# Kernel tuning notes

Hardware: AMD Instinct MI355X
Metric: run time of the kernel (lower is better)

## Reference

```python
import jax, jax.numpy as jnp
import numpy as np

DIM = 512
QK_DIM = 128
HIDDEN = 1024


def setup_inputs() -> dict:
    key = jax.random.key(0)
    ks = jax.random.split(key, 8)
    b, n = 4, 4096
    x = jax.random.normal(ks[0], (b, n, DIM), dtype=jnp.float32)
    # nn.Linear(dim, hidden*2)
    w_hidden = jax.random.normal(ks[1], (DIM, 2 * HIDDEN), dtype=jnp.float32) / np.sqrt(DIM)
    b_hidden = jnp.zeros((2 * HIDDEN,), dtype=jnp.float32)
    # nn.Linear(dim, qk_dim, bias=False)
    w_qk = jax.random.normal(ks[2], (DIM, QK_DIM), dtype=jnp.float32) / np.sqrt(DIM)
    # OffsetScale params (gamma init 1, beta init 0; randomize slightly for a nontrivial test)
    q_gamma = 1.0 + 0.02 * jax.random.normal(ks[3], (QK_DIM,), dtype=jnp.float32)
    q_beta = 0.02 * jax.random.normal(ks[4], (QK_DIM,), dtype=jnp.float32)
    k_gamma = 1.0 + 0.02 * jax.random.normal(ks[5], (QK_DIM,), dtype=jnp.float32)
    k_beta = 0.02 * jax.random.normal(ks[6], (QK_DIM,), dtype=jnp.float32)
    # nn.Linear(hidden, dim)
    w_out = jax.random.normal(ks[7], (HIDDEN, DIM), dtype=jnp.float32) / np.sqrt(HIDDEN)
    b_out = jnp.zeros((DIM,), dtype=jnp.float32)
    return {
        "x": x,
        "w_hidden": w_hidden, "b_hidden": b_hidden,
        "w_qk": w_qk,
        "q_gamma": q_gamma, "q_beta": q_beta,
        "k_gamma": k_gamma, "k_beta": k_beta,
        "w_out": w_out, "b_out": b_out,
    }


def reference(x, w_hidden, b_hidden, w_qk, q_gamma, q_beta, k_gamma, k_beta, w_out, b_out):
    scale = QK_DIM ** -0.5
    # to_hidden -> chunk into v, gate (NOTE: source applies no activation here)
    hid = jnp.einsum('bnd,dh->bnh', x, w_hidden) + b_hidden  # [b, n, 2*hidden]
    v, gate = jnp.split(hid, 2, axis=-1)                     # each [b, n, hidden]
    qk = jnp.einsum('bnd,de->bne', x, w_qk)                  # [b, n, qk_dim]
    q = qk * q_gamma + q_beta
    k = qk * k_gamma + k_beta
    sim = jnp.einsum('bid,bjd->bij', q, k) * scale           # [b, n, n]
    attn = jnp.square(jax.nn.relu(sim))                      # ReLU^2, no softmax
    out = jnp.einsum('bij,bjh->bih', attn, v)                # [b, n, hidden]
    out = out * gate
    out = jnp.einsum('bnh,hd->bnd', out, w_out) + b_out      # [b, n, dim]
    return out + x  # add_residual=True
```

## Files before the change

### kernel.cpp

```cpp
#include <hip/hip_runtime.h>
#include <hip/hip_bf16.h>

typedef __attribute__((ext_vector_type(8))) short bf16x8;
typedef __attribute__((ext_vector_type(4))) float f32x4;
typedef unsigned short u16;

__device__ __forceinline__ u16 f2b(float f) {
  __hip_bfloat16 h = __float2bfloat16(f);
  return __builtin_bit_cast(unsigned short, h);
}
__device__ __forceinline__ float b2f(u16 u) {
  __hip_bfloat16 h = __builtin_bit_cast(__hip_bfloat16, u);
  return __bfloat162float(h);
}

#define BAR() __builtin_amdgcn_s_barrier()
#define LGKM0() do { asm volatile("s_waitcnt lgkmcnt(0)" ::: "memory"); __builtin_amdgcn_sched_barrier(0); } while (0)
#define LGKM4() do { asm volatile("s_waitcnt lgkmcnt(4)" ::: "memory"); __builtin_amdgcn_sched_barrier(0); } while (0)
#define LGKM8() do { asm volatile("s_waitcnt lgkmcnt(8)" ::: "memory"); __builtin_amdgcn_sched_barrier(0); } while (0)
#define VMCNT4() asm volatile("s_waitcnt vmcnt(4)" ::: "memory")
#define VMCNT2() asm volatile("s_waitcnt vmcnt(2)" ::: "memory")
#define VMCNT0() asm volatile("s_waitcnt vmcnt(0)" ::: "memory")

#define EPI_HID 0
#define EPI_QK 1
#define EPI_ATTN 2
#define EPI_PV 3
#define EPI_OUT 4

__device__ __forceinline__ void stage_tile(char* sbase, const char* gbase, int ld_bytes, int tid) {
#pragma unroll
  for (int i = 0; i < 4; ++i) {
    int o = (i * 256 + tid) * 16;
    int row = o >> 7;
    int cb = o & 127;
    int scb = cb ^ ((row & 7) << 4);
    const char* src = gbase + (long)row * ld_bytes + scb;
    __builtin_amdgcn_global_load_lds((const __attribute__((address_space(1))) void*)src,
                                     (__attribute__((address_space(3))) void*)(sbase + o),
                                     16, 0, 0);
  }
}

template <int EPI>
__global__ __launch_bounds__(256, 2) void gemm_tn(
    const char* Ab, const char* Bb, long sAbat, long sBbat,
    int lda_b, int ldb_b, int nkt,
    u16* o0, u16* o1,
    const float* a0, const float* a1, const float* a2, const float* a3,
    float* fout, const float* xres) {
  __shared__ __align__(16) char lds[32768];
  char* sA = lds;
  char* sB = lds + 16384;
  const int tid = threadIdx.x;
  const int lane = tid & 63;
  const int wave = tid >> 6;
  const int wm = wave >> 1, wn = wave & 1;
  const int l16 = lane & 15, lq = lane >> 4;
  const int bat = blockIdx.z;
  const int row0 = blockIdx.y * 128;
  const int col0 = blockIdx.x * 128;

  const char* Abase = Ab + (long)bat * sAbat + (long)row0 * lda_b;
  const char* Bbase = Bb + (long)bat * sBbat + (long)col0 * ldb_b;

  f32x4 acc[4][4];
#pragma unroll
  for (int i = 0; i < 4; ++i)
#pragma unroll
    for (int j = 0; j < 4; ++j) acc[i][j] = (f32x4){0.f, 0.f, 0.f, 0.f};

  for (int kt = 0; kt < nkt; ++kt) {
    stage_tile(sA, Abase + (long)kt * 128, lda_b, tid);
    stage_tile(sB, Bbase + (long)kt * 128, ldb_b, tid);
    __syncthreads();
#pragma unroll
    for (int kk = 0; kk < 2; ++kk) {
      bf16x8 af[4], bfr[4];
#pragma unroll
      for (int mf = 0; mf < 4; ++mf) {
        int r = wm * 64 + mf * 16 + l16;
        int kb = kk * 64 + lq * 16;
        af[mf] = *(const bf16x8*)(sA + r * 128 + (kb ^ ((r & 7) << 4)));
      }
#pragma unroll
      for (int nf = 0; nf < 4; ++nf) {
        int r = wn * 64 + nf * 16 + l16;
        int kb = kk * 64 + lq * 16;
        bfr[nf] = *(const bf16x8*)(sB + r * 128 + (kb ^ ((r & 7) << 4)));
      }
#pragma unroll
      for (int mf = 0; mf < 4; ++mf)
#pragma unroll
        for (int nf = 0; nf < 4; ++nf)
          acc[mf][nf] = __builtin_amdgcn_mfma_f32_16x16x32_bf16(af[mf], bfr[nf], acc[mf][nf], 0, 0, 0);
    }
    __syncthreads();
  }

#pragma unroll
  for (int mf = 0; mf < 4; ++mf) {
#pragma unroll
    for (int nf = 0; nf < 4; ++nf) {
      const int row = row0 + wm * 64 + mf * 16 + lq * 4;
      const int col = col0 + wn * 64 + nf * 16 + l16;
      f32x4 v = acc[mf][nf];
      if constexpr (EPI == EPI_QK) {
        float qg = a0[col], qbt = a1[col], kg = a2[col], kbt = a3[col];
#pragma unroll
        for (int i = 0; i < 4; ++i) {
          float t = v[i];
          o0[(size_t)(row + i) * 128 + col] = f2b(t * qg + qbt);
          o1[(size_t)(row + i) * 128 + col] = f2b(t * kg + kbt);
        }
      }
    }
  }
}

__device__ __forceinline__ void stage_half(char* sbase, const char* gbase, long ld, int tid) {
#pragma unroll
  for (int i = 0; i < 2; ++i) {
    int o = (i * 512 + tid) * 16;
    int row = o >> 7;
    int cb = o & 127;
    int scb = cb ^ ((row & 7) << 4);
    const char* src = gbase + (long)row * ld + scb;
    __builtin_amdgcn_global_load_lds((const __attribute__((address_space(1))) void*)src,
                                     (__attribute__((address_space(3))) void*)(sbase + o),
                                     16, 0, 0);
  }
}

template <int EPI>
__global__ __launch_bounds__(512, 2) void gemm256(
    const char* Ab, const char* Bb, long sAbat, long sBbat,
    long lda, long ldb, int nkt, int nx,
    u16* o0, u16* o1,
    const float* a0, float* fout, const float* xres) {
  extern __shared__ __align__(16) char lds[];
  const int tid = threadIdx.x;
  const int lane = tid & 63;
  const int wave = tid >> 6;
  const int wm = wave >> 2;
  const int wn = wave & 3;
  const int l16 = lane & 15, lq = lane >> 4;
  const int bat = blockIdx.y;

  const int nwg = gridDim.x;
  const int qq = nwg >> 3;
  const int fid = blockIdx.x;
  const int swz = (fid & 7) * qq + (fid >> 3);
  const int row0 = (swz / nx) * 256;
  const int col0 = (swz % nx) * 256;

  const char* gA = Ab + (long)bat * sAbat + (long)row0 * lda;
  const char* gB = Bb + (long)bat * sBbat + (long)col0 * ldb;

  f32x4 acc[8][4];
#pragma unroll
  for (int i = 0; i < 8; ++i)
#pragma unroll
    for (int j = 0; j < 4; ++j) acc[i][j] = (f32x4){0.f, 0.f, 0.f, 0.f};

  const int kmask = (l16 & 7) << 4;
  const int kb0 = (lq * 16) ^ kmask;
  const int kb1 = (64 + lq * 16) ^ kmask;
  const int rB = (wn & 1) * 64;

  stage_half(lds + 32768, gB, ldb, tid);
  stage_half(lds + 32768 + 16384, gB + 128 * ldb, ldb, tid);
  stage_half(lds, gA, lda, tid);
  stage_half(lds + 16384, gA + 128 * lda, lda, tid);
  if (nkt > 1) {
    stage_half(lds + 65536 + 32768, gB + 128, ldb, tid);
    stage_half(lds + 65536 + 32768 + 16384, gB + 128 * ldb + 128, ldb, tid);
    VMCNT4();
  } else {
    VMCNT0();
  }
  BAR();

  bf16x8 af0[4], af1[4], afp0[4], afp1[4], bfr0[4], bfr1[4];
  {
    const char* myA = lds + wm * 16384;
    const char* myB = lds + 32768 + (wn >> 1) * 16384;
#pragma unroll
    for (int nf = 0; nf < 4; ++nf)
      bfr0[nf] = *(const bf16x8*)(myB + (rB + nf * 16 + l16) * 128 + kb0);
#pragma unroll
    for (int mf = 0; mf < 4; ++mf)
      af0[mf] = *(const bf16x8*)(myA + (mf * 16 + l16) * 128 + kb0);
  }

  for (int t = 0; t < nkt; ++t) {
    const char* bufc = lds + (t & 1) * 65536;
    const char* bufn = lds + ((t + 1) & 1) * 65536;
    const char* myA = bufc + wm * 16384;
    const char* myB = bufc + 32768 + (wn >> 1) * 16384;
    const char* nA = bufn + wm * 16384;
    const char* nB = bufn + 32768 + (wn >> 1) * 16384;
    char* stA = (char*)bufn;
    char* stB = (char*)bufc + 32768;
    const bool sA_ok = (t + 1) < nkt;
    const bool sB_ok = (t + 2) < nkt;

#pragma unroll
    for (int nf = 0; nf < 4; ++nf)
      bfr1[nf] = *(const bf16x8*)(myB + (rB + nf * 16 + l16) * 128 + kb1);
#pragma unroll
    for (int mf = 0; mf < 4; ++mf)
      af1[mf] = *(const bf16x8*)(myA + (mf * 16 + l16) * 128 + kb1);
    if (sA_ok) stage_half(stA, gA + (long)(t + 1) * 128, lda, tid);
    LGKM8();
    __builtin_amdgcn_s_setprio(1);
#pragma unroll
    for (int mf = 0; mf < 4; ++mf)
#pragma unroll
      for (int nf = 0; nf < 4; ++nf)
        acc[mf][nf] = __builtin_amdgcn_mfma_f32_16x16x32_bf16(af0[mf], bfr0[nf], acc[mf][nf], 0, 0, 0);
    __builtin_amdgcn_s_setprio(0);

#pragma unroll
    for (int mf = 0; mf < 4; ++mf)
      afp0[mf] = *(const bf16x8*)(myA + (64 + mf * 16 + l16) * 128 + kb0);
    if (sA_ok) stage_half(stA + 16384, gA + 128 * lda + (long)(t + 1) * 128, lda, tid);
    LGKM4();
    __builtin_amdgcn_s_setprio(1);
#pragma unroll
    for (int mf = 0; mf < 4; ++mf)
#pragma unroll
      for (int nf = 0; nf < 4; ++nf)
        acc[mf][nf] = __builtin_amdgcn_mfma_f32_16x16x32_bf16(af1[mf], bfr1[nf], acc[mf][nf], 0, 0, 0);
    __builtin_amdgcn_s_setprio(0);
    BAR();

#pragma unroll
    for (int mf = 0; mf < 4; ++mf)
      afp1[mf] = *(const bf16x8*)(myA + (64 + mf * 16 + l16) * 128 + kb1);
    if (sB_ok) stage_half(stB, gB + (long)(t + 2) * 128, ldb, tid);
    LGKM4();
    __builtin_amdgcn_s_setprio(1);
#pragma unroll
    for (int mf = 0; mf < 4; ++mf)
#pragma unroll
      for (int nf = 0; nf < 4; ++nf)
        acc[4 + mf][nf] = __builtin_amdgcn_mfma_f32_16x16x32_bf16(afp0[mf], bfr0[nf], acc[4 + mf][nf], 0, 0, 0);
    __builtin_amdgcn_s_setprio(0);
    if (sA_ok) {
      if (sB_ok) { VMCNT2(); } else { VMCNT0(); }
      BAR();
    }

    if (sA_ok) {
#pragma unroll
      for (int nf = 0; nf < 4; ++nf)
        bfr0[nf] = *(const bf16x8*)(nB + (rB + nf * 16 + l16) * 128 + kb0);
#pragma unroll
      for (int mf = 0; mf < 4; ++mf)
        af0[mf] = *(const bf16x8*)(nA + (mf * 16 + l16) * 128 + kb0);
    }
    if (sB_ok) stage_half(stB + 16384, gB + 128 * ldb + (long)(t + 2) * 128, ldb, tid);
    if (sA_ok) { LGKM8(); } else { LGKM0(); }
    __builtin_amdgcn_s_setprio(1);
#pragma unroll
    for (int mf = 0; mf < 4; ++mf)
#pragma unroll
      for (int nf = 0; nf < 4; ++nf)
        acc[4 + mf][nf] = __builtin_amdgcn_mfma_f32_16x16x32_bf16(afp1[mf], bfr1[nf], acc[4 + mf][nf], 0, 0, 0);
    __builtin_amdgcn_s_setprio(0);
    BAR();
  }

#pragma unroll
  for (int mi = 0; mi < 8; ++mi) {
#pragma unroll
    for (int ni = 0; ni < 4; ++ni) {
      const int row = row0 + wm * 128 + mi * 16 + lq * 4;
      const int col = col0 + wn * 64 + ni * 16 + l16;
      f32x4 v = acc[mi][ni];
      if constexpr (EPI == EPI_HID) {
        float bias = a0[col];
        u16* dst = (col < 1024) ? (o0 + (size_t)col * 16384 + row)
                                : (o1 + (size_t)(col - 1024) * 16384 + row);
        *(ushort4*)dst = make_ushort4(f2b(v.x + bias), f2b(v.y + bias), f2b(v.z + bias), f2b(v.w + bias));
      } else if constexpr (EPI == EPI_ATTN) {
        const float scale = 0.088388347648318447f;
        u16* dst = o0 + (size_t)bat * 4096 * 4096;
#pragma unroll
        for (int i = 0; i < 4; ++i) {
          float t = v[i] * scale;
          t = t > 0.f ? t * t : 0.f;
          dst[(size_t)(row + i) * 4096 + col] = f2b(t);
        }
      } else if constexpr (EPI == EPI_PV) {
        const u16* gt = o1 + (size_t)col * 16384 + (size_t)bat * 4096 + row;
        ushort4 g = *(const ushort4*)gt;
        u16* dst = o0 + (size_t)bat * 4096 * 1024;
        dst[(size_t)(row + 0) * 1024 + col] = f2b(v.x * b2f(g.x));
        dst[(size_t)(row + 1) * 1024 + col] = f2b(v.y * b2f(g.y));
        dst[(size_t)(row + 2) * 1024 + col] = f2b(v.z * b2f(g.z));
        dst[(size_t)(row + 3) * 1024 + col] = f2b(v.w * b2f(g.w));
      } else if constexpr (EPI == EPI_OUT) {
        float bias = a0[col];
#pragma unroll
        for (int i = 0; i < 4; ++i)
          fout[(size_t)(row + i) * 512 + col] = v[i] + bias + xres[(size_t)(row + i) * 512 + col];
      }
    }
  }
}

__global__ void conv_b(const float* in, u16* out, int n) {
  int i = (blockIdx.x * blockDim.x + threadIdx.x) * 4;
  if (i >= n) return;
  float4 f = *(const float4*)(in + i);
  *(ushort4*)(out + i) = make_ushort4(f2b(f.x), f2b(f.y), f2b(f.z), f2b(f.w));
}

__global__ void transpose_b(const float* in, u16* out, int R, int C) {
  int o = blockIdx.x * blockDim.x + threadIdx.x;
  if (o >= R * C) return;
  int c = o / R, r = o - c * R;
  out[o] = f2b(in[(size_t)r * C + c]);
}

extern "C" void kernel_launch(void* const* d_in, const int* in_sizes, int n_in,
                              void* d_out, int out_size, void* d_ws, size_t ws_size,
                              hipStream_t stream) {
  const float* x = (const float*)d_in[0];
  const float* w_hidden = (const float*)d_in[1];
  const float* b_hidden = (const float*)d_in[2];
  const float* w_qk = (const float*)d_in[3];
  const float* q_gamma = (const float*)d_in[4];
  const float* q_beta = (const float*)d_in[5];
  const float* k_gamma = (const float*)d_in[6];
  const float* k_beta = (const float*)d_in[7];
  const float* w_out = (const float*)d_in[8];
  const float* b_out = (const float*)d_in[9];
  float* out = (float*)d_out;

  char* ws = (char*)d_ws;
  size_t off = 0;
  auto alloc = [&](size_t bytes) { char* p = ws + off; off += (bytes + 255) & ~255ull; return p; };
  u16* xb     = (u16*)alloc(16384ull * 512 * 2);
  u16* wh_t   = (u16*)alloc(2048ull * 512 * 2);
  u16* wqk_t  = (u16*)alloc(128ull * 512 * 2);
  u16* wout_t = (u16*)alloc(512ull * 1024 * 2);
  u16* v_t    = (u16*)alloc(1024ull * 16384 * 2);
  u16* g_t    = (u16*)alloc(1024ull * 16384 * 2);
  u16* qb_a   = (u16*)alloc(16384ull * 128 * 2);
  u16* kb_a   = (u16*)alloc(16384ull * 128 * 2);
  u16* attnb  = (u16*)alloc(4ull * 4096 * 4096 * 2);
  u16* out1b  = (u16*)alloc(16384ull * 1024 * 2);

  (void)hipFuncSetAttribute((const void*)gemm256<EPI_HID>, hipFuncAttributeMaxDynamicSharedMemorySize, 131072);
  (void)hipFuncSetAttribute((const void*)gemm256<EPI_ATTN>, hipFuncAttributeMaxDynamicSharedMemorySize, 131072);
  (void)hipFuncSetAttribute((const void*)gemm256<EPI_PV>, hipFuncAttributeMaxDynamicSharedMemorySize, 131072);
  (void)hipFuncSetAttribute((const void*)gemm256<EPI_OUT>, hipFuncAttributeMaxDynamicSharedMemorySize, 131072);

  conv_b<<<(16384 * 512 / 4 + 255) / 256, 256, 0, stream>>>(x, xb, 16384 * 512);
  transpose_b<<<(512 * 2048 + 255) / 256, 256, 0, stream>>>(w_hidden, wh_t, 512, 2048);
  transpose_b<<<(512 * 128 + 255) / 256, 256, 0, stream>>>(w_qk, wqk_t, 512, 128);
  transpose_b<<<(1024 * 512 + 255) / 256, 256, 0, stream>>>(w_out, wout_t, 1024, 512);

  gemm256<EPI_HID><<<dim3(512, 1), 512, 131072, stream>>>(
      (const char*)xb, (const char*)wh_t, 0, 0, 1024, 1024, 8, 8,
      v_t, g_t, b_hidden, nullptr, nullptr);
  gemm_tn<EPI_QK><<<dim3(1, 128, 1), 256, 0, stream>>>(
      (const char*)xb, (const char*)wqk_t, 0, 0, 1024, 1024, 8,
      qb_a, kb_a, q_gamma, q_beta, k_gamma, k_beta, nullptr, nullptr);
  gemm256<EPI_ATTN><<<dim3(256, 4), 512, 131072, stream>>>(
      (const char*)qb_a, (const char*)kb_a, 4096ll * 256, 4096ll * 256, 256, 256, 2, 16,
      attnb, nullptr, nullptr, nullptr, nullptr);
  gemm256<EPI_PV><<<dim3(64, 4), 512, 131072, stream>>>(
      (const char*)attnb, (const char*)v_t, 4096ll * 8192, 8192, 8192, 32768, 64, 4,
      out1b, g_t, nullptr, nullptr, nullptr);
  gemm256<EPI_OUT><<<dim3(128, 1), 512, 131072, stream>>>(
      (const char*)out1b, (const char*)wout_t, 0, 0, 2048, 2048, 16, 2,
      nullptr, nullptr, b_out, out, x);
}
```

Measured before the change: 343.7 us.

## Switch 256-tile GEMM to 32x32x16 MFMA and move output projection to gemm_tn

Rewrites the main 256x256 GEMM inner loop to use 32x32x16 bf16 MFMA instructions with 16-float accumulators instead of 16x16x32, which halves the instruction count per tile and changes the fragment layout and epilogue indexing. It also moves the final output-projection GEMM to the smaller gemm_tn kernel with a new EPI_OUT epilogue, giving more workgroups for that small-N problem. The risks are new LDS bank-conflict patterns from the different fragment layout and changed register pressure.

```diff
diff --git a/kernel.cpp b/kernel.cpp
--- a/kernel.cpp
+++ b/kernel.cpp
@@ -3,6 +3,7 @@
 
 typedef __attribute__((ext_vector_type(8))) short bf16x8;
 typedef __attribute__((ext_vector_type(4))) float f32x4;
+typedef __attribute__((ext_vector_type(16))) float f32x16;
 typedef unsigned short u16;
 
 __device__ __forceinline__ u16 f2b(float f) {
@@ -113,6 +114,11 @@
           o0[(size_t)(row + i) * 128 + col] = f2b(t * qg + qbt);
           o1[(size_t)(row + i) * 128 + col] = f2b(t * kg + kbt);
         }
+      } else if constexpr (EPI == EPI_OUT) {
+        float bias = a0[col];
+#pragma unroll
+        for (int i = 0; i < 4; ++i)
+          fout[(size_t)(row + i) * 512 + col] = v[i] + bias + xres[(size_t)(row + i) * 512 + col];
       }
     }
   }
@@ -144,7 +150,7 @@
   const int wave = tid >> 6;
   const int wm = wave >> 2;
   const int wn = wave & 3;
-  const int l16 = lane & 15, lq = lane >> 4;
+  const int l31 = lane & 31, hi = lane >> 5;
   const int bat = blockIdx.y;
 
   const int nwg = gridDim.x;
@@ -157,15 +163,18 @@
   const char* gA = Ab + (long)bat * sAbat + (long)row0 * lda;
   const char* gB = Bb + (long)bat * sBbat + (long)col0 * ldb;
 
-  f32x4 acc[8][4];
-#pragma unroll
-  for (int i = 0; i < 8; ++i)
-#pragma unroll
-    for (int j = 0; j < 4; ++j) acc[i][j] = (f32x4){0.f, 0.f, 0.f, 0.f};
-
-  const int kmask = (l16 & 7) << 4;
-  const int kb0 = (lq * 16) ^ kmask;
-  const int kb1 = (64 + lq * 16) ^ kmask;
+  f32x16 acc[4][2];
+#pragma unroll
+  for (int i = 0; i < 4; ++i)
+#pragma unroll
+    for (int j = 0; j < 2; ++j)
+#pragma unroll
+      for (int e = 0; e < 16; ++e) acc[i][j][e] = 0.f;
+
+  const int kmask = (l31 & 7) << 4;
+  int kb[4];
+#pragma unroll
+  for (int ks = 0; ks < 4; ++ks) kb[ks] = (ks * 32 + hi * 16) ^ kmask;
   const int rB = (wn & 1) * 64;
 
   stage_half(lds + 32768, gB, ldb, tid);
@@ -186,11 +195,15 @@
     const char* myA = lds + wm * 16384;
     const char* myB = lds + 32768 + (wn >> 1) * 16384;
 #pragma unroll
-    for (int nf = 0; nf < 4; ++nf)
-      bfr0[nf] = *(const bf16x8*)(myB + (rB + nf * 16 + l16) * 128 + kb0);
-#pragma unroll
-    for (int mf = 0; mf < 4; ++mf)
-      af0[mf] = *(const bf16x8*)(myA + (mf * 16 + l16) * 128 + kb0);
+    for (int ni = 0; ni < 2; ++ni)
+#pragma unroll
+      for (int ki = 0; ki < 2; ++ki)
+        bfr0[ni * 2 + ki] = *(const bf16x8*)(myB + (rB + ni * 32 + l31) * 128 + kb[ki]);
+#pragma unroll
+    for (int mi = 0; mi < 2; ++mi)
+#pragma unroll
+      for (int ki = 0; ki < 2; ++ki)
+        af0[mi * 2 + ki] = *(const bf16x8*)(myA + (mi * 32 + l31) * 128 + kb[ki]);
   }
 
   for (int t = 0; t < nkt; ++t) {
@@ -206,46 +219,60 @@
     const bool sB_ok = (t + 2) < nkt;
 
 #pragma unroll
-    for (int nf = 0; nf < 4; ++nf)
-      bfr1[nf] = *(const bf16x8*)(myB + (rB + nf * 16 + l16) * 128 + kb1);
-#pragma unroll
-    for (int mf = 0; mf < 4; ++mf)
-      af1[mf] = *(const bf16x8*)(myA + (mf * 16 + l16) * 128 + kb1);
+    for (int ni = 0; ni < 2; ++ni)
+#pragma unroll
+      for (int ki = 0; ki < 2; ++ki)
+        bfr1[ni * 2 + ki] = *(const bf16x8*)(myB + (rB + ni * 32 + l31) * 128 + kb[2 + ki]);
+#pragma unroll
+    for (int mi = 0; mi < 2; ++mi)
+#pragma unroll
+      for (int ki = 0; ki < 2; ++ki)
+        af1[mi * 2 + ki] = *(const bf16x8*)(myA + (mi * 32 + l31) * 128 + kb[2 + ki]);
     if (sA_ok) stage_half(stA, gA + (long)(t + 1) * 128, lda, tid);
     LGKM8();
     __builtin_amdgcn_s_setprio(1);
 #pragma unroll
-    for (int mf = 0; mf < 4; ++mf)
-#pragma unroll
-      for (int nf = 0; nf < 4; ++nf)
-        acc[mf][nf] = __builtin_amdgcn_mfma_f32_16x16x32_bf16(af0[mf], bfr0[nf], acc[mf][nf], 0, 0, 0);
+    for (int ki = 0; ki < 2; ++ki)
+#pragma unroll
+      for (int mi = 0; mi < 2; ++mi)
+#pragma unroll
+        for (int ni = 0; ni < 2; ++ni)
+          acc[mi][ni] = __builtin_amdgcn_mfma_f32_32x32x16_bf16(af0[mi * 2 + ki], bfr0[ni * 2 + ki], acc[mi][ni], 0, 0, 0);
     __builtin_amdgcn_s_setprio(0);
 
 #pragma unroll
-    for (int mf = 0; mf < 4; ++mf)
-      afp0[mf] = *(const bf16x8*)(myA + (64 + mf * 16 + l16) * 128 + kb0);
+    for (int mi = 0; mi < 2; ++mi)
+#pragma unroll
+      for (int ki = 0; ki < 2; ++ki)
+        afp0[mi * 2 + ki] = *(const bf16x8*)(myA + ((mi + 2) * 32 + l31) * 128 + kb[ki]);
     if (sA_ok) stage_half(stA + 16384, gA + 128 * lda + (long)(t + 1) * 128, lda, tid);
     LGKM4();
     __builtin_amdgcn_s_setprio(1);
 #pragma unroll
-    for (int mf = 0; mf < 4; ++mf)
-#pragma unroll
-      for (int nf = 0; nf < 4; ++nf)
-        acc[mf][nf] = __builtin_amdgcn_mfma_f32_16x16x32_bf16(af1[mf], bfr1[nf], acc[mf][nf], 0, 0, 0);
+    for (int ki = 0; ki < 2; ++ki)
+#pragma unroll
+      for (int mi = 0; mi < 2; ++mi)
+#pragma unroll
+        for (int ni = 0; ni < 2; ++ni)
+          acc[mi][ni] = __builtin_amdgcn_mfma_f32_32x32x16_bf16(af1[mi * 2 + ki], bfr1[ni * 2 + ki], acc[mi][ni], 0, 0, 0);
     __builtin_amdgcn_s_setprio(0);
     BAR();
 
 #pragma unroll
-    for (int mf = 0; mf < 4; ++mf)
-      afp1[mf] = *(const bf16x8*)(myA + (64 + mf * 16 + l16) * 128 + kb1);
+    for (int mi = 0; mi < 2; ++mi)
+#pragma unroll
+      for (int ki = 0; ki < 2; ++ki)
+        afp1[mi * 2 + ki] = *(const bf16x8*)(myA + ((mi + 2) * 32 + l31) * 128 + kb[2 + ki]);
     if (sB_ok) stage_half(stB, gB + (long)(t + 2) * 128, ldb, tid);
     LGKM4();
     __builtin_amdgcn_s_setprio(1);
 #pragma unroll
-    for (int mf = 0; mf < 4; ++mf)
-#pragma unroll
-      for (int nf = 0; nf < 4; ++nf)
-        acc[4 + mf][nf] = __builtin_amdgcn_mfma_f32_16x16x32_bf16(afp0[mf], bfr0[nf], acc[4 + mf][nf], 0, 0, 0);
+    for (int ki = 0; ki < 2; ++ki)
+#pragma unroll
+      for (int mi = 0; mi < 2; ++mi)
+#pragma unroll
+        for (int ni = 0; ni < 2; ++ni)
+          acc[2 + mi][ni] = __builtin_amdgcn_mfma_f32_32x32x16_bf16(afp0[mi * 2 + ki], bfr0[ni * 2 + ki], acc[2 + mi][ni], 0, 0, 0);
     __builtin_amdgcn_s_setprio(0);
     if (sA_ok) {
       if (sB_ok) { VMCNT2(); } else { VMCNT0(); }
@@ -254,58 +281,69 @@
 
     if (sA_ok) {
 #pragma unroll
-      for (int nf = 0; nf < 4; ++nf)
-        bfr0[nf] = *(const bf16x8*)(nB + (rB + nf * 16 + l16) * 128 + kb0);
-#pragma unroll
-      for (int mf = 0; mf < 4; ++mf)
-        af0[mf] = *(const bf16x8*)(nA + (mf * 16 + l16) * 128 + kb0);
+      for (int ni = 0; ni < 2; ++ni)
+#pragma unroll
+        for (int ki = 0; ki < 2; ++ki)
+          bfr0[ni * 2 + ki] = *(const bf16x8*)(nB + (rB + ni * 32 + l31) * 128 + kb[ki]);
+#pragma unroll
+      for (int mi = 0; mi < 2; ++mi)
+#pragma unroll
+        for (int ki = 0; ki < 2; ++ki)
+          af0[mi * 2 + ki] = *(const bf16x8*)(nA + (mi * 32 + l31) * 128 + kb[ki]);
     }
     if (sB_ok) stage_half(stB + 16384, gB + 128 * ldb + (long)(t + 2) * 128, ldb, tid);
     if (sA_ok) { LGKM8(); } else { LGKM0(); }
     __builtin_amdgcn_s_setprio(1);
 #pragma unroll
-    for (int mf = 0; mf < 4; ++mf)
-#pragma unroll
-      for (int nf = 0; nf < 4; ++nf)
-        acc[4 + mf][nf] = __builtin_amdgcn_mfma_f32_16x16x32_bf16(afp1[mf], bfr1[nf], acc[4 + mf][nf], 0, 0, 0);
+    for (int ki = 0; ki < 2; ++ki)
+#pragma unroll
+      for (int mi = 0; mi < 2; ++mi)
+#pragma unroll
+        for (int ni = 0; ni < 2; ++ni)
+          acc[2 + mi][ni] = __builtin_amdgcn_mfma_f32_32x32x16_bf16(afp1[mi * 2 + ki], bfr1[ni * 2 + ki], acc[2 + mi][ni], 0, 0, 0);
     __builtin_amdgcn_s_setprio(0);
     BAR();
   }
 
 #pragma unroll
-  for (int mi = 0; mi < 8; ++mi) {
-#pragma unroll
-    for (int ni = 0; ni < 4; ++ni) {
-      const int row = row0 + wm * 128 + mi * 16 + lq * 4;
-      const int col = col0 + wn * 64 + ni * 16 + l16;
-      f32x4 v = acc[mi][ni];
+  for (int mi = 0; mi < 4; ++mi) {
+#pragma unroll
+    for (int ni = 0; ni < 2; ++ni) {
+      f32x16 v = acc[mi][ni];
+      const int col = col0 + wn * 64 + ni * 32 + l31;
+      const int rowb = row0 + wm * 128 + mi * 32 + 4 * hi;
       if constexpr (EPI == EPI_HID) {
         float bias = a0[col];
-        u16* dst = (col < 1024) ? (o0 + (size_t)col * 16384 + row)
-                                : (o1 + (size_t)(col - 1024) * 16384 + row);
-        *(ushort4*)dst = make_ushort4(f2b(v.x + bias), f2b(v.y + bias), f2b(v.z + bias), f2b(v.w + bias));
+        u16* dst = (col < 1024) ? (o0 + (size_t)col * 16384)
+                                : (o1 + (size_t)(col - 1024) * 16384);
+#pragma unroll
+        for (int q = 0; q < 4; ++q) {
+          ushort4 pk = make_ushort4(f2b(v[4 * q + 0] + bias), f2b(v[4 * q + 1] + bias),
+                                    f2b(v[4 * q + 2] + bias), f2b(v[4 * q + 3] + bias));
+          *(ushort4*)(dst + rowb + 8 * q) = pk;
+        }
       } else if constexpr (EPI == EPI_ATTN) {
         const float scale = 0.088388347648318447f;
         u16* dst = o0 + (size_t)bat * 4096 * 4096;
 #pragma unroll
-        for (int i = 0; i < 4; ++i) {
-          float t = v[i] * scale;
-          t = t > 0.f ? t * t : 0.f;
-          dst[(size_t)(row + i) * 4096 + col] = f2b(t);
+        for (int q = 0; q < 4; ++q)
+#pragma unroll
+          for (int j = 0; j < 4; ++j) {
+            float tt = v[4 * q + j] * scale;
+            tt = tt > 0.f ? tt * tt : 0.f;
+            dst[(size_t)(rowb + 8 * q + j) * 4096 + col] = f2b(tt);
+          }
+      } else if constexpr (EPI == EPI_PV) {
+        const u16* gt = o1 + (size_t)col * 16384 + (size_t)bat * 4096;
+        u16* dst = o0 + (size_t)bat * 4096 * 1024;
+#pragma unroll
+        for (int q = 0; q < 4; ++q) {
+          ushort4 g = *(const ushort4*)(gt + rowb + 8 * q);
+          dst[(size_t)(rowb + 8 * q + 0) * 1024 + col] = f2b(v[4 * q + 0] * b2f(g.x));
+          dst[(size_t)(rowb + 8 * q + 1) * 1024 + col] = f2b(v[4 * q + 1] * b2f(g.y));
+          dst[(size_t)(rowb + 8 * q + 2) * 1024 + col] = f2b(v[4 * q + 2] * b2f(g.z));
+          dst[(size_t)(rowb + 8 * q + 3) * 1024 + col] = f2b(v[4 * q + 3] * b2f(g.w));
         }
-      } else if constexpr (EPI == EPI_PV) {
-        const u16* gt = o1 + (size_t)col * 16384 + (size_t)bat * 4096 + row;
-        ushort4 g = *(const ushort4*)gt;
-        u16* dst = o0 + (size_t)bat * 4096 * 1024;
-        dst[(size_t)(row + 0) * 1024 + col] = f2b(v.x * b2f(g.x));
-        dst[(size_t)(row + 1) * 1024 + col] = f2b(v.y * b2f(g.y));
-        dst[(size_t)(row + 2) * 1024 + col] = f2b(v.z * b2f(g.z));
-        dst[(size_t)(row + 3) * 1024 + col] = f2b(v.w * b2f(g.w));
-      } else if constexpr (EPI == EPI_OUT) {
-        float bias = a0[col];
-#pragma unroll
-        for (int i = 0; i < 4; ++i)
-          fout[(size_t)(row + i) * 512 + col] = v[i] + bias + xres[(size_t)(row + i) * 512 + col];
       }
     }
   }
@@ -357,7 +395,6 @@
   (void)hipFuncSetAttribute((const void*)gemm256<EPI_HID>, hipFuncAttributeMaxDynamicSharedMemorySize, 131072);
   (void)hipFuncSetAttribute((const void*)gemm256<EPI_ATTN>, hipFuncAttributeMaxDynamicSharedMemorySize, 131072);
   (void)hipFuncSetAttribute((const void*)gemm256<EPI_PV>, hipFuncAttributeMaxDynamicSharedMemorySize, 131072);
-  (void)hipFuncSetAttribute((const void*)gemm256<EPI_OUT>, hipFuncAttributeMaxDynamicSharedMemorySize, 131072);
 
   conv_b<<<(16384 * 512 / 4 + 255) / 256, 256, 0, stream>>>(x, xb, 16384 * 512);
   transpose_b<<<(512 * 2048 + 255) / 256, 256, 0, stream>>>(w_hidden, wh_t, 512, 2048);
@@ -376,7 +413,7 @@
   gemm256<EPI_PV><<<dim3(64, 4), 512, 131072, stream>>>(
       (const char*)attnb, (const char*)v_t, 4096ll * 8192, 8192, 8192, 32768, 64, 4,
       out1b, g_t, nullptr, nullptr, nullptr);
-  gemm256<EPI_OUT><<<dim3(128, 1), 512, 131072, stream>>>(
-      (const char*)out1b, (const char*)wout_t, 0, 0, 2048, 2048, 16, 2,
-      nullptr, nullptr, b_out, out, x);
-}
+  gemm_tn<EPI_OUT><<<dim3(4, 128, 1), 256, 0, stream>>>(
+      (const char*)out1b, (const char*)wout_t, 0, 0, 2048, 2048, 16,
+      nullptr, nullptr, b_out, nullptr, nullptr, nullptr, out, x);
+}
```

Measured after the change: 320.8 us. 1.07x faster.

## Fuse attention score and PV GEMMs into one kernel, drop attn matrix

Applied to the files above, without the earlier changes.

Replaces the separate QK^T (writing a 4x4096x4096 bf16 attention matrix) and attn@V GEMMs with one fused kernel. It computes ReLU^2 scores per 64-key tile into LDS and immediately multiplies them by V, double-buffering K and V tiles. This removes roughly 128MB of global write and reread traffic. The cost is that each of the four hidden-dim tiles recomputes QK^T for its query block. The output projection also moves from the 256-tile kernel to the smaller gemm_tn kernel with a new EPI_OUT epilogue.

```diff
diff --git a/kernel.cpp b/kernel.cpp
--- a/kernel.cpp
+++ b/kernel.cpp
@@ -24,8 +24,6 @@
 
 #define EPI_HID 0
 #define EPI_QK 1
-#define EPI_ATTN 2
-#define EPI_PV 3
 #define EPI_OUT 4
 
 __device__ __forceinline__ void stage_tile(char* sbase, const char* gbase, int ld_bytes, int tid) {
@@ -113,6 +111,11 @@
           o0[(size_t)(row + i) * 128 + col] = f2b(t * qg + qbt);
           o1[(size_t)(row + i) * 128 + col] = f2b(t * kg + kbt);
         }
+      } else if constexpr (EPI == EPI_OUT) {
+        float bias = a0[col];
+#pragma unroll
+        for (int i = 0; i < 4; ++i)
+          fout[(size_t)(row + i) * 512 + col] = v[i] + bias + xres[(size_t)(row + i) * 512 + col];
       }
     }
   }
@@ -284,29 +287,171 @@
         u16* dst = (col < 1024) ? (o0 + (size_t)col * 16384 + row)
                                 : (o1 + (size_t)(col - 1024) * 16384 + row);
         *(ushort4*)dst = make_ushort4(f2b(v.x + bias), f2b(v.y + bias), f2b(v.z + bias), f2b(v.w + bias));
-      } else if constexpr (EPI == EPI_ATTN) {
-        const float scale = 0.088388347648318447f;
-        u16* dst = o0 + (size_t)bat * 4096 * 4096;
+      }
+    }
+  }
+}
+
+__device__ __forceinline__ void stage_k64(char* s, const char* g, int tid) {
+#pragma unroll
+  for (int i = 0; i < 2; ++i) {
+    int o = (i * 512 + tid) * 16;
+    int row = o >> 8;
+    int cb = o & 255;
+    int scb = cb ^ ((row & 7) << 4);
+    __builtin_amdgcn_global_load_lds((const __attribute__((address_space(1))) void*)(g + (long)row * 256 + scb),
+                                     (__attribute__((address_space(3))) void*)(s + o), 16, 0, 0);
+  }
+}
+__device__ __forceinline__ void stage_v256(char* s, const char* g, int tid) {
+#pragma unroll
+  for (int i = 0; i < 4; ++i) {
+    int o = (i * 512 + tid) * 16;
+    int row = o >> 7;
+    int cb = o & 127;
+    int scb = cb ^ ((row & 7) << 4);
+    __builtin_amdgcn_global_load_lds((const __attribute__((address_space(1))) void*)(g + (long)row * 32768 + scb),
+                                     (__attribute__((address_space(3))) void*)(s + o), 16, 0, 0);
+  }
+}
+
+__global__ __launch_bounds__(512, 2) void attnpv(
+    const char* qb, const char* kb, const char* vt,
+    const u16* gt, u16* out1) {
+  extern __shared__ __align__(16) char lds[];
+  const int tid = threadIdx.x;
+  const int lane = tid & 63;
+  const int wave = tid >> 6;
+  const int wq = wave >> 2, wh = wave & 3;
+  const int l16 = lane & 15, lq = lane >> 4;
+  const int bat = blockIdx.y;
+
+  const int nwg = gridDim.x;
+  const int qq = nwg >> 3;
+  const int fid = blockIdx.x;
+  const int swz = (fid & 7) * qq + (fid >> 3);
+  const int qt = swz >> 2;
+  const int ht = swz & 3;
+  const int q0 = qt * 256, h0 = ht * 256;
+
+  char* kbuf0 = lds;
+  char* kbuf1 = lds + 16384;
+  char* vbuf0 = lds + 32768;
+  char* vbuf1 = lds + 65536;
+  char* pbuf = lds + 98304;
+
+  const char* kb_g = kb + ((size_t)bat * 4096) * 256;
+  const char* vt_g = vt + (size_t)h0 * 32768 + ((size_t)bat * 4096) * 2;
+
+  const int kmask = (l16 & 7) << 4;
+
+  bf16x8 qf[2][4];
+  {
+    const char* qg = qb + ((size_t)(bat * 4096 + q0 + wave * 32)) * 256;
+#pragma unroll
+    for (int mf = 0; mf < 2; ++mf)
+#pragma unroll
+      for (int kk = 0; kk < 4; ++kk)
+        qf[mf][kk] = *(const bf16x8*)(qg + (size_t)(mf * 16 + l16) * 256 + (kk * 64 + lq * 16));
+  }
+
+  f32x4 acc[8][4];
+#pragma unroll
+  for (int i = 0; i < 8; ++i)
+#pragma unroll
+    for (int j = 0; j < 4; ++j) acc[i][j] = (f32x4){0.f, 0.f, 0.f, 0.f};
+
+  stage_k64(kbuf0, kb_g, tid);
+  stage_v256(vbuf0, vt_g, tid);
+  VMCNT0();
+  BAR();
+
+  const float scale = 0.088388347648318447f;
+
+  for (int jt = 0; jt < 64; ++jt) {
+    char* kc = (jt & 1) ? kbuf1 : kbuf0;
+    char* vc = (jt & 1) ? vbuf1 : vbuf0;
+    char* kn = (jt & 1) ? kbuf0 : kbuf1;
+    char* vn = (jt & 1) ? vbuf0 : vbuf1;
+    if (jt + 1 < 64) {
+      stage_k64(kn, kb_g + (size_t)(jt + 1) * 16384, tid);
+      stage_v256(vn, vt_g + (size_t)(jt + 1) * 128, tid);
+    }
+
+    f32x4 sacc[2][4];
+#pragma unroll
+    for (int i = 0; i < 2; ++i)
+#pragma unroll
+      for (int j = 0; j < 4; ++j) sacc[i][j] = (f32x4){0.f, 0.f, 0.f, 0.f};
+#pragma unroll
+    for (int kh = 0; kh < 2; ++kh) {
+      bf16x8 kfr[8];
+#pragma unroll
+      for (int nf = 0; nf < 4; ++nf)
+#pragma unroll
+        for (int ki = 0; ki < 2; ++ki)
+          kfr[nf * 2 + ki] = *(const bf16x8*)(kc + (nf * 16 + l16) * 256 + (((kh * 2 + ki) * 64 + lq * 16) ^ kmask));
+      __builtin_amdgcn_s_setprio(1);
+#pragma unroll
+      for (int ki = 0; ki < 2; ++ki)
+#pragma unroll
+        for (int mf = 0; mf < 2; ++mf)
+#pragma unroll
+          for (int nf = 0; nf < 4; ++nf)
+            sacc[mf][nf] = __builtin_amdgcn_mfma_f32_16x16x32_bf16(qf[mf][kh * 2 + ki], kfr[nf * 2 + ki], sacc[mf][nf], 0, 0, 0);
+      __builtin_amdgcn_s_setprio(0);
+    }
+
+#pragma unroll
+    for (int mf = 0; mf < 2; ++mf)
+#pragma unroll
+      for (int nf = 0; nf < 4; ++nf)
 #pragma unroll
         for (int i = 0; i < 4; ++i) {
-          float t = v[i] * scale;
+          int qloc = wave * 32 + mf * 16 + lq * 4 + i;
+          float t = sacc[mf][nf][i] * scale;
           t = t > 0.f ? t * t : 0.f;
-          dst[(size_t)(row + i) * 4096 + col] = f2b(t);
+          int byte = qloc * 128 + (((nf * 16 + l16) * 2) ^ ((qloc & 7) << 4));
+          *(u16*)(pbuf + byte) = f2b(t);
         }
-      } else if constexpr (EPI == EPI_PV) {
-        const u16* gt = o1 + (size_t)col * 16384 + (size_t)bat * 4096 + row;
-        ushort4 g = *(const ushort4*)gt;
-        u16* dst = o0 + (size_t)bat * 4096 * 1024;
-        dst[(size_t)(row + 0) * 1024 + col] = f2b(v.x * b2f(g.x));
-        dst[(size_t)(row + 1) * 1024 + col] = f2b(v.y * b2f(g.y));
-        dst[(size_t)(row + 2) * 1024 + col] = f2b(v.z * b2f(g.z));
-        dst[(size_t)(row + 3) * 1024 + col] = f2b(v.w * b2f(g.w));
-      } else if constexpr (EPI == EPI_OUT) {
-        float bias = a0[col];
-#pragma unroll
-        for (int i = 0; i < 4; ++i)
-          fout[(size_t)(row + i) * 512 + col] = v[i] + bias + xres[(size_t)(row + i) * 512 + col];
-      }
+    LGKM0();
+    BAR();
+
+#pragma unroll
+    for (int ki = 0; ki < 2; ++ki) {
+      bf16x8 pa[8], vf[4];
+#pragma unroll
+      for (int mf = 0; mf < 8; ++mf)
+        pa[mf] = *(const bf16x8*)(pbuf + (wq * 128 + mf * 16 + l16) * 128 + ((ki * 64 + lq * 16) ^ kmask));
+#pragma unroll
+      for (int nf = 0; nf < 4; ++nf)
+        vf[nf] = *(const bf16x8*)(vc + (wh * 64 + nf * 16 + l16) * 128 + ((ki * 64 + lq * 16) ^ kmask));
+      __builtin_amdgcn_s_setprio(1);
+#pragma unroll
+      for (int mf = 0; mf < 8; ++mf)
+#pragma unroll
+        for (int nf = 0; nf < 4; ++nf)
+          acc[mf][nf] = __builtin_amdgcn_mfma_f32_16x16x32_bf16(pa[mf], vf[nf], acc[mf][nf], 0, 0, 0);
+      __builtin_amdgcn_s_setprio(0);
+    }
+    VMCNT0();
+    BAR();
+  }
+
+#pragma unroll
+  for (int mi = 0; mi < 8; ++mi) {
+#pragma unroll
+    for (int ni = 0; ni < 4; ++ni) {
+      const int row = q0 + wq * 128 + mi * 16 + lq * 4;
+      const int col = h0 + wh * 64 + ni * 16 + l16;
+      f32x4 v = acc[mi][ni];
+      const u16* gp = gt + (size_t)col * 16384 + (size_t)bat * 4096 + row;
+      ushort4 g = *(const ushort4*)gp;
+      u16* dst = out1 + (size_t)bat * 4096 * 1024;
+      dst[(size_t)(row + 0) * 1024 + col] = f2b(v.x * b2f(g.x));
+      dst[(size_t)(row + 1) * 1024 + col] = f2b(v.y * b2f(g.y));
+      dst[(size_t)(row + 2) * 1024 + col] = f2b(v.z * b2f(g.z));
+      dst[(size_t)(row + 3) * 1024 + col] = f2b(v.w * b2f(g.w));
     }
   }
 }
@@ -351,13 +496,10 @@
   u16* g_t    = (u16*)alloc(1024ull * 16384 * 2);
   u16* qb_a   = (u16*)alloc(16384ull * 128 * 2);
   u16* kb_a   = (u16*)alloc(16384ull * 128 * 2);
-  u16* attnb  = (u16*)alloc(4ull * 4096 * 4096 * 2);
   u16* out1b  = (u16*)alloc(16384ull * 1024 * 2);
 
   (void)hipFuncSetAttribute((const void*)gemm256<EPI_HID>, hipFuncAttributeMaxDynamicSharedMemorySize, 131072);
-  (void)hipFuncSetAttribute((const void*)gemm256<EPI_ATTN>, hipFuncAttributeMaxDynamicSharedMemorySize, 131072);
-  (void)hipFuncSetAttribute((const void*)gemm256<EPI_PV>, hipFuncAttributeMaxDynamicSharedMemorySize, 131072);
-  (void)hipFuncSetAttribute((const void*)gemm256<EPI_OUT>, hipFuncAttributeMaxDynamicSharedMemorySize, 131072);
+  (void)hipFuncSetAttribute((const void*)attnpv, hipFuncAttributeMaxDynamicSharedMemorySize, 131072);
 
   conv_b<<<(16384 * 512 / 4 + 255) / 256, 256, 0, stream>>>(x, xb, 16384 * 512);
   transpose_b<<<(512 * 2048 + 255) / 256, 256, 0, stream>>>(w_hidden, wh_t, 512, 2048);
@@ -370,13 +512,9 @@
   gemm_tn<EPI_QK><<<dim3(1, 128, 1), 256, 0, stream>>>(
       (const char*)xb, (const char*)wqk_t, 0, 0, 1024, 1024, 8,
       qb_a, kb_a, q_gamma, q_beta, k_gamma, k_beta, nullptr, nullptr);
-  gemm256<EPI_ATTN><<<dim3(256, 4), 512, 131072, stream>>>(
-      (const char*)qb_a, (const char*)kb_a, 4096ll * 256, 4096ll * 256, 256, 256, 2, 16,
-      attnb, nullptr, nullptr, nullptr, nullptr);
-  gemm256<EPI_PV><<<dim3(64, 4), 512, 131072, stream>>>(
-      (const char*)attnb, (const char*)v_t, 4096ll * 8192, 8192, 8192, 32768, 64, 4,
-      out1b, g_t, nullptr, nullptr, nullptr);
-  gemm256<EPI_OUT><<<dim3(128, 1), 512, 131072, stream>>>(
-      (const char*)out1b, (const char*)wout_t, 0, 0, 2048, 2048, 16, 2,
-      nullptr, nullptr, b_out, out, x);
-}
+  attnpv<<<dim3(64, 4), 512, 131072, stream>>>(
+      (const char*)qb_a, (const char*)kb_a, (const char*)v_t, g_t, out1b);
+  gemm_tn<EPI_OUT><<<dim3(4, 128, 1), 256, 0, stream>>>(
+      (const char*)out1b, (const char*)wout_t, 0, 0, 2048, 2048, 16,
+      nullptr, nullptr, b_out, nullptr, nullptr, nullptr, out, x);
+}
```

Measured after the change: 470.2 us. 36.8% more time.
